# Kernel optimization log

Measured on AMD Instinct MI355X. Metric: run time of the kernel, lower is better.

Reference implementation:

```python
import jax, jax.numpy as jnp
import numpy as np

B, N, DIM = 2, 2048, 1024
NUM_HEADS = 16
EFF = NUM_HEADS // 2          # 8 effective heads
HD = DIM // NUM_HEADS         # 64
LAMBDA_INIT = 0.8
EPS = 1e-5


def setup_inputs() -> dict:
    key = jax.random.key(0)
    ks = jax.random.split(key, 16)
    s = 0.02
    return {
        "x":  jax.random.normal(ks[0], (B, N, DIM), dtype=jnp.float32),
        "Wq": jax.random.normal(ks[1], (DIM, DIM), dtype=jnp.float32) * s,
        "bq": jnp.zeros((DIM,), dtype=jnp.float32),
        "Wk": jax.random.normal(ks[2], (DIM, DIM), dtype=jnp.float32) * s,
        "bk": jnp.zeros((DIM,), dtype=jnp.float32),
        "Wv": jax.random.normal(ks[3], (DIM, DIM), dtype=jnp.float32) * s,
        "bv": jnp.zeros((DIM,), dtype=jnp.float32),
        "Wo": jax.random.normal(ks[4], (DIM, DIM), dtype=jnp.float32) * s,
        "bo": jnp.zeros((DIM,), dtype=jnp.float32),
        "norm_w": jnp.ones((2 * HD,), dtype=jnp.float32),
        "lq1": jax.random.normal(ks[5], (HD,), dtype=jnp.float32) * 0.1,
        "lk1": jax.random.normal(ks[6], (HD,), dtype=jnp.float32) * 0.1,
        "lq2": jax.random.normal(ks[7], (HD,), dtype=jnp.float32) * 0.1,
        "lk2": jax.random.normal(ks[8], (HD,), dtype=jnp.float32) * 0.1,
    }


def reference(x, Wq, bq, Wk, bk, Wv, bv, Wo, bo, norm_w, lq1, lk1, lq2, lk2):
    scale = HD ** -0.5
    # projections (torch Linear: y = x @ W.T + b)
    q = (x @ Wq.T + bq).reshape(B, N, NUM_HEADS, HD).transpose(0, 2, 1, 3) * scale  # [B,2E,N,hd]
    k = (x @ Wk.T + bk).reshape(B, N, NUM_HEADS, HD).transpose(0, 2, 1, 3)          # [B,2E,N,hd]
    v = (x @ Wv.T + bv).reshape(B, N, EFF, 2 * HD).transpose(0, 2, 1, 3)            # [B,E,N,2hd]

    scores = jnp.einsum('bhqd,bhkd->bhqk', q, k)              # [B,2E,N,N]
    probs = jax.nn.softmax(scores, axis=-1)
    probs = probs.reshape(B, EFF, 2, N, N)                    # pair consecutive heads

    lam = jnp.exp(jnp.sum(lq1 * lk1)) - jnp.exp(jnp.sum(lq2 * lk2)) + LAMBDA_INIT
    diff = probs[:, :, 0] - lam * probs[:, :, 1]              # [B,E,N,N]

    out = jnp.einsum('behk,bekd->behd'.replace('e','h').replace('hh','h') if False else 'bhqk,bhkd->bhqd', diff, v)  # [B,E,N,2hd]
    # headwise RMSNorm over last dim (2*hd)
    out = out * jax.lax.rsqrt(jnp.mean(out * out, axis=-1, keepdims=True) + EPS) * norm_w
    out = out * (1.0 - LAMBDA_INIT)

    out = out.transpose(0, 2, 1, 3).reshape(B, N, DIM)
    return out @ Wo.T + bo
```

## Files before the change

### kernel.cpp

```cpp
#include <hip/hip_runtime.h>
#include <hip/hip_bf16.h>

#define B_   2
#define N_   2048
#define DIM_ 1024
#define HD_  64
#define DV_  128

typedef __bf16 bf16;
typedef __bf16 bf16x8 __attribute__((ext_vector_type(8)));
typedef __bf16 bf16x4 __attribute__((ext_vector_type(4)));
typedef float  floatx4 __attribute__((ext_vector_type(4)));

#if __has_builtin(__builtin_amdgcn_exp2f)
#define EXP2(x) __builtin_amdgcn_exp2f(x)
#else
#define EXP2(x) exp2f(x)
#endif

#define QSCALE 0.1803368801111244f

__device__ __forceinline__ void async16(const void* g, void* l) {
  __builtin_amdgcn_global_load_lds(
      (__attribute__((address_space(1))) void*)g,
      (__attribute__((address_space(3))) void*)l, 16, 0, 0);
}

__global__ void convert_kernel(const float* __restrict__ x,
                               const float* __restrict__ wq,
                               const float* __restrict__ wk,
                               const float* __restrict__ wv,
                               const float* __restrict__ wo,
                               bf16* __restrict__ dst) {
  const int NX = B_ * N_ * DIM_;
  const int NW = DIM_ * DIM_;
  int i = (blockIdx.x * 256 + threadIdx.x) * 4;
  const float* src;
  int off;
  if (i < NX) { src = x; off = i; }
  else {
    int j = i - NX;
    int w = j >> 20;
    off = j & (NW - 1);
    src = (w == 0) ? wq : (w == 1) ? wk : (w == 2) ? wv : wo;
  }
  float4 v = *(const float4*)(src + off);
  bf16x4 o = { (bf16)v.x, (bf16)v.y, (bf16)v.z, (bf16)v.w };
  *(bf16x4*)(dst + i) = o;
}

__global__ void lam_kernel(const float* __restrict__ lq1, const float* __restrict__ lk1,
                           const float* __restrict__ lq2, const float* __restrict__ lk2,
                           float* __restrict__ lam_out) {
  int l = threadIdx.x;
  float a = lq1[l] * lk1[l];
  float b = lq2[l] * lk2[l];
  for (int m = 1; m < 64; m <<= 1) {
    a += __shfl_xor(a, m, 64);
    b += __shfl_xor(b, m, 64);
  }
  if (l == 0) *lam_out = __expf(a) - __expf(b) + 0.8f;
}

__global__ __launch_bounds__(256) void proj_kernel(
    const bf16* __restrict__ xb, const bf16* __restrict__ wall,
    const float* __restrict__ bq, const float* __restrict__ bk,
    const float* __restrict__ bv,
    bf16* __restrict__ qo, bf16* __restrict__ ko, bf16* __restrict__ vt) {
  __shared__ __align__(16) bf16 At[128 * 64];
  __shared__ __align__(16) bf16 Bt[128 * 64];
  const int tid = threadIdx.x, lane = tid & 63, w = tid >> 6;
  const int tm = blockIdx.x, tn = blockIdx.y, z = blockIdx.z;
  const int quad = lane >> 4, l15 = lane & 15;
  const int wm = (w >> 1) * 64, wn = (w & 1) * 64;
  const bf16* Ab = xb + (long)tm * 128 * DIM_;
  const bf16* Bb = wall + (long)z * (DIM_ * DIM_) + (long)tn * 128 * DIM_;
  floatx4 zero = {0.f, 0.f, 0.f, 0.f};
  floatx4 acc[4][4];
#pragma unroll
  for (int i = 0; i < 4; ++i)
#pragma unroll
    for (int j = 0; j < 4; ++j) acc[i][j] = zero;

  for (int kb = 0; kb < DIM_ / 64; ++kb) {
    for (int idx = tid; idx < 1024; idx += 256) {
      int row = idx >> 3, ch = idx & 7, g = ch ^ (row & 7);
      async16(Ab + row * DIM_ + kb * 64 + g * 8, (char*)At + (idx - lane) * 16);
      async16(Bb + row * DIM_ + kb * 64 + g * 8, (char*)Bt + (idx - lane) * 16);
    }
    __syncthreads();
#pragma unroll
    for (int ks = 0; ks < 2; ++ks) {
      bf16x8 af[4], bfm[4];
#pragma unroll
      for (int mt = 0; mt < 4; ++mt) {
        int r = wm + mt * 16 + l15;
        af[mt] = *(const bf16x8*)&At[r * 64 + ((ks * 4 + quad) ^ (r & 7)) * 8];
      }
#pragma unroll
      for (int nt = 0; nt < 4; ++nt) {
        int r = wn + nt * 16 + l15;
        bfm[nt] = *(const bf16x8*)&Bt[r * 64 + ((ks * 4 + quad) ^ (r & 7)) * 8];
      }
#pragma unroll
      for (int mt = 0; mt < 4; ++mt)
#pragma unroll
        for (int nt = 0; nt < 4; ++nt)
          acc[mt][nt] = __builtin_amdgcn_mfma_f32_16x16x32_bf16(
              af[mt], bfm[nt], acc[mt][nt], 0, 0, 0);
    }
    __syncthreads();
  }
#pragma unroll
  for (int mt = 0; mt < 4; ++mt)
#pragma unroll
    for (int nt = 0; nt < 4; ++nt)
#pragma unroll
      for (int r = 0; r < 4; ++r) {
        int grow = tm * 128 + wm + mt * 16 + quad * 4 + r;
        int gcol = tn * 128 + wn + nt * 16 + l15;
        float v = acc[mt][nt][r];
        if (z == 0) {
          qo[(long)grow * DIM_ + gcol] = (bf16)((v + bq[gcol]) * QSCALE);
        } else if (z == 1) {
          ko[(long)grow * DIM_ + gcol] = (bf16)(v + bk[gcol]);
        } else {
          int bb = grow >> 11, key = grow & (N_ - 1);
          int e = gcol >> 7, d = gcol & 127;
          vt[(((long)(bb * 8 + e)) * DV_ + d) * N_ + key] = (bf16)(v + bv[gcol]);
        }
      }
}

__global__ __launch_bounds__(256) void attn_kernel(
    const bf16* __restrict__ qb, const bf16* __restrict__ kbuf,
    const bf16* __restrict__ vt, float* __restrict__ O) {
  __shared__ __align__(16) bf16 Qt[64 * 64];
  __shared__ __align__(16) bf16 Kt[64 * 64];
  __shared__ __align__(16) bf16 Pt[64 * 64];
  __shared__ __align__(16) bf16 Vt[128 * 64];
  const int tid = threadIdx.x, lane = tid & 63, w = tid >> 6;
  const int qt = blockIdx.x, h = blockIdx.y, b = blockIdx.z, e = h >> 1;
  const int quad = lane >> 4, l15 = lane & 15;
  floatx4 zero = {0.f, 0.f, 0.f, 0.f};

  for (int idx = tid; idx < 512; idx += 256) {
    int row = idx >> 3, ch = idx & 7, g = ch ^ (row & 7);
    async16(qb + ((long)(b * N_ + qt * 64 + row)) * DIM_ + h * 64 + g * 8,
            (char*)Qt + (idx - lane) * 16);
  }
  __syncthreads();
  bf16x8 qf[2];
  {
    int ar = w * 16 + l15;
    qf[0] = *(const bf16x8*)&Qt[ar * 64 + ((quad) ^ (ar & 7)) * 8];
    qf[1] = *(const bf16x8*)&Qt[ar * 64 + ((4 + quad) ^ (ar & 7)) * 8];
  }

  floatx4 acc[8];
#pragma unroll
  for (int i = 0; i < 8; ++i) acc[i] = zero;
  float lpart[4] = {0.f, 0.f, 0.f, 0.f};

  for (int kt = 0; kt < N_ / 64; ++kt) {
    for (int idx = tid; idx < 512; idx += 256) {
      int row = idx >> 3, ch = idx & 7, g = ch ^ (row & 7);
      async16(kbuf + ((long)(b * N_ + kt * 64 + row)) * DIM_ + h * 64 + g * 8,
              (char*)Kt + (idx - lane) * 16);
    }
    for (int idx = tid; idx < 1024; idx += 256) {
      int row = idx >> 3, ch = idx & 7, g = ch ^ (row & 7);
      async16(vt + ((long)((b * 8 + e) * DV_ + row)) * N_ + kt * 64 + g * 8,
              (char*)Vt + (idx - lane) * 16);
    }
    __syncthreads();

    floatx4 s[4];
#pragma unroll
    for (int nt = 0; nt < 4; ++nt) s[nt] = zero;
#pragma unroll
    for (int ks = 0; ks < 2; ++ks) {
#pragma unroll
      for (int nt = 0; nt < 4; ++nt) {
        int br = nt * 16 + l15;
        bf16x8 bfm = *(const bf16x8*)&Kt[br * 64 + ((ks * 4 + quad) ^ (br & 7)) * 8];
        s[nt] = __builtin_amdgcn_mfma_f32_16x16x32_bf16(qf[ks], bfm, s[nt], 0, 0, 0);
      }
    }

#pragma unroll
    for (int r = 0; r < 4; ++r) {
      float p0 = EXP2(s[0][r]);
      float p1 = EXP2(s[1][r]);
      float p2 = EXP2(s[2][r]);
      float p3 = EXP2(s[3][r]);
      lpart[r] += (p0 + p1) + (p2 + p3);
      int row = w * 16 + quad * 4 + r;
      int k0 = l15;
      Pt[row * 64 + ((k0 >> 3) ^ (row & 7)) * 8 + (k0 & 7)] = (bf16)p0;
      int k1 = 16 + l15;
      Pt[row * 64 + ((k1 >> 3) ^ (row & 7)) * 8 + (k1 & 7)] = (bf16)p1;
      int k2 = 32 + l15;
      Pt[row * 64 + ((k2 >> 3) ^ (row & 7)) * 8 + (k2 & 7)] = (bf16)p2;
      int k3 = 48 + l15;
      Pt[row * 64 + ((k3 >> 3) ^ (row & 7)) * 8 + (k3 & 7)] = (bf16)p3;
    }

#pragma unroll
    for (int ks = 0; ks < 2; ++ks) {
      int ar = w * 16 + l15;
      bf16x8 af = *(const bf16x8*)&Pt[ar * 64 + ((ks * 4 + quad) ^ (ar & 7)) * 8];
#pragma unroll
      for (int dt = 0; dt < 8; ++dt) {
        int br = dt * 16 + l15;
        bf16x8 bfm = *(const bf16x8*)&Vt[br * 64 + ((ks * 4 + quad) ^ (br & 7)) * 8];
        acc[dt] = __builtin_amdgcn_mfma_f32_16x16x32_bf16(af, bfm, acc[dt], 0, 0, 0);
      }
    }
    __syncthreads();
  }

  float inv[4];
#pragma unroll
  for (int r = 0; r < 4; ++r) {
    float ls = lpart[r];
#pragma unroll
    for (int msk = 1; msk < 16; msk <<= 1) ls += __shfl_xor(ls, msk, 16);
    inv[r] = 1.0f / ls;
  }
#pragma unroll
  for (int dt = 0; dt < 8; ++dt)
#pragma unroll
    for (int r = 0; r < 4; ++r) {
      int q = qt * 64 + w * 16 + quad * 4 + r;
      int d = dt * 16 + l15;
      O[(((long)(b * 16 + h)) * N_ + q) * DV_ + d] = acc[dt][r] * inv[r];
    }
}

__global__ void combine_kernel(const float* __restrict__ O, const float* __restrict__ lamp,
                               const float* __restrict__ norm_w, bf16* __restrict__ ao) {
  int bid = blockIdx.x;
  int e = bid & 7, n = (bid >> 3) & (N_ - 1), b = bid >> 14;
  int lane = threadIdx.x;
  float lam = *lamp;
  const float* o1 = O + (((long)(b * 16 + 2 * e)) * N_ + n) * DV_;
  const float* o2 = O + (((long)(b * 16 + 2 * e + 1)) * N_ + n) * DV_;
  float d0 = o1[lane] - lam * o2[lane];
  float d1 = o1[lane + 64] - lam * o2[lane + 64];
  float ss = d0 * d0 + d1 * d1;
  for (int m = 1; m < 64; m <<= 1) ss += __shfl_xor(ss, m, 64);
  float r = rsqrtf(ss * (1.0f / 128.0f) + 1e-5f);
  float y0 = d0 * r * norm_w[lane] * 0.2f;
  float y1 = d1 * r * norm_w[lane + 64] * 0.2f;
  bf16* dst = ao + ((long)(b * N_ + n)) * DIM_ + e * DV_;
  dst[lane] = (bf16)y0;
  dst[lane + 64] = (bf16)y1;
}

__global__ __launch_bounds__(256) void out_gemm(
    const bf16* __restrict__ ab, const bf16* __restrict__ wo,
    const float* __restrict__ bo, float* __restrict__ out) {
  __shared__ __align__(16) bf16 At[128 * 64];
  __shared__ __align__(16) bf16 Bt[128 * 64];
  const int tid = threadIdx.x, lane = tid & 63, w = tid >> 6;
  const int tm = blockIdx.x, tn = blockIdx.y;
  const int quad = lane >> 4, l15 = lane & 15;
  const int wm = (w >> 1) * 64, wn = (w & 1) * 64;
  const bf16* Ab = ab + (long)tm * 128 * DIM_;
  const bf16* Bb = wo + (long)tn * 128 * DIM_;
  floatx4 zero = {0.f, 0.f, 0.f, 0.f};
  floatx4 acc[4][4];
#pragma unroll
  for (int i = 0; i < 4; ++i)
#pragma unroll
    for (int j = 0; j < 4; ++j) acc[i][j] = zero;

  for (int kb = 0; kb < DIM_ / 64; ++kb) {
    for (int idx = tid; idx < 1024; idx += 256) {
      int row = idx >> 3, ch = idx & 7, g = ch ^ (row & 7);
      async16(Ab + row * DIM_ + kb * 64 + g * 8, (char*)At + (idx - lane) * 16);
      async16(Bb + row * DIM_ + kb * 64 + g * 8, (char*)Bt + (idx - lane) * 16);
    }
    __syncthreads();
#pragma unroll
    for (int ks = 0; ks < 2; ++ks) {
      bf16x8 af[4], bfm[4];
#pragma unroll
      for (int mt = 0; mt < 4; ++mt) {
        int r = wm + mt * 16 + l15;
        af[mt] = *(const bf16x8*)&At[r * 64 + ((ks * 4 + quad) ^ (r & 7)) * 8];
      }
#pragma unroll
      for (int nt = 0; nt < 4; ++nt) {
        int r = wn + nt * 16 + l15;
        bfm[nt] = *(const bf16x8*)&Bt[r * 64 + ((ks * 4 + quad) ^ (r & 7)) * 8];
      }
#pragma unroll
      for (int mt = 0; mt < 4; ++mt)
#pragma unroll
        for (int nt = 0; nt < 4; ++nt)
          acc[mt][nt] = __builtin_amdgcn_mfma_f32_16x16x32_bf16(
              af[mt], bfm[nt], acc[mt][nt], 0, 0, 0);
    }
    __syncthreads();
  }
#pragma unroll
  for (int mt = 0; mt < 4; ++mt)
#pragma unroll
    for (int nt = 0; nt < 4; ++nt)
#pragma unroll
      for (int r = 0; r < 4; ++r) {
        int grow = tm * 128 + wm + mt * 16 + quad * 4 + r;
        int gcol = tn * 128 + wn + nt * 16 + l15;
        out[(long)grow * DIM_ + gcol] = acc[mt][nt][r] + bo[gcol];
      }
}

extern "C" void kernel_launch(void* const* d_in, const int* in_sizes, int n_in,
                              void* d_out, int out_size, void* d_ws, size_t ws_size,
                              hipStream_t stream) {
  const float* x    = (const float*)d_in[0];
  const float* Wq   = (const float*)d_in[1];
  const float* bq   = (const float*)d_in[2];
  const float* Wk   = (const float*)d_in[3];
  const float* bk   = (const float*)d_in[4];
  const float* Wv   = (const float*)d_in[5];
  const float* bv   = (const float*)d_in[6];
  const float* Wo   = (const float*)d_in[7];
  const float* bo   = (const float*)d_in[8];
  const float* nw   = (const float*)d_in[9];
  const float* lq1  = (const float*)d_in[10];
  const float* lk1  = (const float*)d_in[11];
  const float* lq2  = (const float*)d_in[12];
  const float* lk2  = (const float*)d_in[13];

  char* ws = (char*)d_ws;
  float* lam = (float*)ws;
  bf16* xb   = (bf16*)(ws + 256);
  bf16* wqb  = xb + 4194304;
  bf16* qb   = wqb + 4 * 1048576;
  bf16* kbuf = qb + 4194304;
  bf16* vtb  = kbuf + 4194304;
  bf16* ab   = vtb + 4194304;
  float* O   = (float*)(ab + 4194304);

  convert_kernel<<<8192, 256, 0, stream>>>(x, Wq, Wk, Wv, Wo, xb);
  lam_kernel<<<1, 64, 0, stream>>>(lq1, lk1, lq2, lk2, lam);
  proj_kernel<<<dim3(32, 8, 3), 256, 0, stream>>>(xb, wqb, bq, bk, bv, qb, kbuf, vtb);
  attn_kernel<<<dim3(32, 16, 2), 256, 0, stream>>>(qb, kbuf, vtb, O);
  combine_kernel<<<32768, 64, 0, stream>>>(O, lam, nw, ab);
  out_gemm<<<dim3(32, 8), 256, 0, stream>>>(ab, wqb + 3 * 1048576, bo, (float*)d_out);
}
```

Baseline: 254.5 us.

## Fuse head-pair attention with differential combine and RMSNorm epilogue

Each attention block now processes both heads of a differential pair, sharing one V tile load across them, and performs the lambda-weighted difference, RMSNorm and scaling in its epilogue, writing bf16 directly to the output-projection input. This removes the fp32 O intermediate write/read and the separate combine kernel launch, and halves V traffic. Q fragments are loaded straight from global, and per-wave P buffers are used. The cost is doubled accumulator registers (two sets of 8 floatx4), which may reduce occupancy, and half as many blocks in the grid.

```diff
diff --git a/kernel.cpp b/kernel.cpp
--- a/kernel.cpp
+++ b/kernel.cpp
@@ -132,130 +132,145 @@
       }
 }
 
-__global__ __launch_bounds__(256) void attn_kernel(
+__global__ __launch_bounds__(256, 2) void attn_kernel(
     const bf16* __restrict__ qb, const bf16* __restrict__ kbuf,
-    const bf16* __restrict__ vt, float* __restrict__ O) {
-  __shared__ __align__(16) bf16 Qt[64 * 64];
-  __shared__ __align__(16) bf16 Kt[64 * 64];
-  __shared__ __align__(16) bf16 Pt[64 * 64];
+    const bf16* __restrict__ vt, const float* __restrict__ lamp,
+    const float* __restrict__ norm_w, bf16* __restrict__ ao) {
+  __shared__ __align__(16) bf16 Kt[2 * 64 * 64];
   __shared__ __align__(16) bf16 Vt[128 * 64];
+  __shared__ __align__(16) bf16 Pt[4 * 16 * 64];
+
   const int tid = threadIdx.x, lane = tid & 63, w = tid >> 6;
-  const int qt = blockIdx.x, h = blockIdx.y, b = blockIdx.z, e = h >> 1;
+  const int qt = blockIdx.x, e = blockIdx.y, b = blockIdx.z;
   const int quad = lane >> 4, l15 = lane & 15;
   floatx4 zero = {0.f, 0.f, 0.f, 0.f};
 
-  for (int idx = tid; idx < 512; idx += 256) {
-    int row = idx >> 3, ch = idx & 7, g = ch ^ (row & 7);
-    async16(qb + ((long)(b * N_ + qt * 64 + row)) * DIM_ + h * 64 + g * 8,
-            (char*)Qt + (idx - lane) * 16);
-  }
-  __syncthreads();
-  bf16x8 qf[2];
-  {
-    int ar = w * 16 + l15;
-    qf[0] = *(const bf16x8*)&Qt[ar * 64 + ((quad) ^ (ar & 7)) * 8];
-    qf[1] = *(const bf16x8*)&Qt[ar * 64 + ((4 + quad) ^ (ar & 7)) * 8];
-  }
-
-  floatx4 acc[8];
-#pragma unroll
-  for (int i = 0; i < 8; ++i) acc[i] = zero;
-  float lpart[4] = {0.f, 0.f, 0.f, 0.f};
+  const int qrow = qt * 64 + w * 16 + l15;
+  const bf16* qrp = qb + (long)(b * N_ + qrow) * DIM_ + e * 128;
+  bf16x8 qf0[2], qf1[2];
+  qf0[0] = *(const bf16x8*)(qrp + quad * 8);
+  qf0[1] = *(const bf16x8*)(qrp + 32 + quad * 8);
+  qf1[0] = *(const bf16x8*)(qrp + 64 + quad * 8);
+  qf1[1] = *(const bf16x8*)(qrp + 96 + quad * 8);
+
+  floatx4 acc0[8], acc1[8];
+#pragma unroll
+  for (int i = 0; i < 8; ++i) { acc0[i] = zero; acc1[i] = zero; }
+  float lp0[4] = {0.f, 0.f, 0.f, 0.f};
+  float lp1[4] = {0.f, 0.f, 0.f, 0.f};
+
+  bf16* Ptw = Pt + w * 1024;
 
   for (int kt = 0; kt < N_ / 64; ++kt) {
-    for (int idx = tid; idx < 512; idx += 256) {
-      int row = idx >> 3, ch = idx & 7, g = ch ^ (row & 7);
-      async16(kbuf + ((long)(b * N_ + kt * 64 + row)) * DIM_ + h * 64 + g * 8,
+#pragma unroll
+    for (int t = 0; t < 4; ++t) {
+      int idx = tid + t * 256;
+      int khl = idx >> 9, row = (idx >> 3) & 63, ch = idx & 7, g = ch ^ (row & 7);
+      async16(kbuf + ((long)(b * N_ + kt * 64 + row)) * DIM_ + (e * 2 + khl) * 64 + g * 8,
               (char*)Kt + (idx - lane) * 16);
     }
-    for (int idx = tid; idx < 1024; idx += 256) {
+#pragma unroll
+    for (int t = 0; t < 4; ++t) {
+      int idx = tid + t * 256;
       int row = idx >> 3, ch = idx & 7, g = ch ^ (row & 7);
       async16(vt + ((long)((b * 8 + e) * DV_ + row)) * N_ + kt * 64 + g * 8,
               (char*)Vt + (idx - lane) * 16);
     }
     __syncthreads();
 
-    floatx4 s[4];
-#pragma unroll
-    for (int nt = 0; nt < 4; ++nt) s[nt] = zero;
-#pragma unroll
-    for (int ks = 0; ks < 2; ++ks) {
-#pragma unroll
-      for (int nt = 0; nt < 4; ++nt) {
-        int br = nt * 16 + l15;
-        bf16x8 bfm = *(const bf16x8*)&Kt[br * 64 + ((ks * 4 + quad) ^ (br & 7)) * 8];
-        s[nt] = __builtin_amdgcn_mfma_f32_16x16x32_bf16(qf[ks], bfm, s[nt], 0, 0, 0);
-      }
-    }
-
+#pragma unroll
+    for (int hl = 0; hl < 2; ++hl) {
+      const bf16* Kh = Kt + hl * 4096;
+      floatx4* acc = hl ? acc1 : acc0;
+      float* lp = hl ? lp1 : lp0;
+
+      floatx4 s[4];
+#pragma unroll
+      for (int nt = 0; nt < 4; ++nt) s[nt] = zero;
+#pragma unroll
+      for (int ks = 0; ks < 2; ++ks) {
+        bf16x8 qf = hl ? qf1[ks] : qf0[ks];
+#pragma unroll
+        for (int nt = 0; nt < 4; ++nt) {
+          int br = nt * 16 + l15;
+          bf16x8 bfm = *(const bf16x8*)&Kh[br * 64 + ((ks * 4 + quad) ^ (br & 7)) * 8];
+          s[nt] = __builtin_amdgcn_mfma_f32_16x16x32_bf16(qf, bfm, s[nt], 0, 0, 0);
+        }
+      }
+
+#pragma unroll
+      for (int r = 0; r < 4; ++r) {
+        float p0 = EXP2(s[0][r]);
+        float p1 = EXP2(s[1][r]);
+        float p2 = EXP2(s[2][r]);
+        float p3 = EXP2(s[3][r]);
+        lp[r] += (p0 + p1) + (p2 + p3);
+        int row = quad * 4 + r;
+        int k0 = l15;
+        Ptw[row * 64 + ((k0 >> 3) ^ (row & 7)) * 8 + (k0 & 7)] = (bf16)p0;
+        int k1 = 16 + l15;
+        Ptw[row * 64 + ((k1 >> 3) ^ (row & 7)) * 8 + (k1 & 7)] = (bf16)p1;
+        int k2 = 32 + l15;
+        Ptw[row * 64 + ((k2 >> 3) ^ (row & 7)) * 8 + (k2 & 7)] = (bf16)p2;
+        int k3 = 48 + l15;
+        Ptw[row * 64 + ((k3 >> 3) ^ (row & 7)) * 8 + (k3 & 7)] = (bf16)p3;
+      }
+
+#pragma unroll
+      for (int ks = 0; ks < 2; ++ks) {
+        bf16x8 af = *(const bf16x8*)&Ptw[l15 * 64 + ((ks * 4 + quad) ^ (l15 & 7)) * 8];
+#pragma unroll
+        for (int dt = 0; dt < 8; ++dt) {
+          int br = dt * 16 + l15;
+          bf16x8 bfm = *(const bf16x8*)&Vt[br * 64 + ((ks * 4 + quad) ^ (br & 7)) * 8];
+          acc[dt] = __builtin_amdgcn_mfma_f32_16x16x32_bf16(af, bfm, acc[dt], 0, 0, 0);
+        }
+      }
+    }
+    __syncthreads();
+  }
+
+  float inv0[4], inv1[4];
+#pragma unroll
+  for (int r = 0; r < 4; ++r) {
+    float a = lp0[r], c = lp1[r];
+#pragma unroll
+    for (int msk = 1; msk < 16; msk <<= 1) {
+      a += __shfl_xor(a, msk, 16);
+      c += __shfl_xor(c, msk, 16);
+    }
+    inv0[r] = 1.0f / a;
+    inv1[r] = 1.0f / c;
+  }
+
+  float lam = *lamp;
+  float ss[4] = {0.f, 0.f, 0.f, 0.f};
+#pragma unroll
+  for (int dt = 0; dt < 8; ++dt)
 #pragma unroll
     for (int r = 0; r < 4; ++r) {
-      float p0 = EXP2(s[0][r]);
-      float p1 = EXP2(s[1][r]);
-      float p2 = EXP2(s[2][r]);
-      float p3 = EXP2(s[3][r]);
-      lpart[r] += (p0 + p1) + (p2 + p3);
-      int row = w * 16 + quad * 4 + r;
-      int k0 = l15;
-      Pt[row * 64 + ((k0 >> 3) ^ (row & 7)) * 8 + (k0 & 7)] = (bf16)p0;
-      int k1 = 16 + l15;
-      Pt[row * 64 + ((k1 >> 3) ^ (row & 7)) * 8 + (k1 & 7)] = (bf16)p1;
-      int k2 = 32 + l15;
-      Pt[row * 64 + ((k2 >> 3) ^ (row & 7)) * 8 + (k2 & 7)] = (bf16)p2;
-      int k3 = 48 + l15;
-      Pt[row * 64 + ((k3 >> 3) ^ (row & 7)) * 8 + (k3 & 7)] = (bf16)p3;
-    }
-
-#pragma unroll
-    for (int ks = 0; ks < 2; ++ks) {
-      int ar = w * 16 + l15;
-      bf16x8 af = *(const bf16x8*)&Pt[ar * 64 + ((ks * 4 + quad) ^ (ar & 7)) * 8];
-#pragma unroll
-      for (int dt = 0; dt < 8; ++dt) {
-        int br = dt * 16 + l15;
-        bf16x8 bfm = *(const bf16x8*)&Vt[br * 64 + ((ks * 4 + quad) ^ (br & 7)) * 8];
-        acc[dt] = __builtin_amdgcn_mfma_f32_16x16x32_bf16(af, bfm, acc[dt], 0, 0, 0);
-      }
-    }
-    __syncthreads();
-  }
-
-  float inv[4];
+      float v = acc0[dt][r] * inv0[r] - lam * (acc1[dt][r] * inv1[r]);
+      acc0[dt][r] = v;
+      ss[r] += v * v;
+    }
+  float rms[4];
 #pragma unroll
   for (int r = 0; r < 4; ++r) {
-    float ls = lpart[r];
-#pragma unroll
-    for (int msk = 1; msk < 16; msk <<= 1) ls += __shfl_xor(ls, msk, 16);
-    inv[r] = 1.0f / ls;
-  }
-#pragma unroll
-  for (int dt = 0; dt < 8; ++dt)
+    float t = ss[r];
+#pragma unroll
+    for (int msk = 1; msk < 16; msk <<= 1) t += __shfl_xor(t, msk, 16);
+    rms[r] = rsqrtf(t * (1.0f / 128.0f) + 1e-5f);
+  }
+#pragma unroll
+  for (int dt = 0; dt < 8; ++dt) {
+    float nwv = norm_w[dt * 16 + l15] * 0.2f;
 #pragma unroll
     for (int r = 0; r < 4; ++r) {
-      int q = qt * 64 + w * 16 + quad * 4 + r;
-      int d = dt * 16 + l15;
-      O[(((long)(b * 16 + h)) * N_ + q) * DV_ + d] = acc[dt][r] * inv[r];
-    }
-}
-
-__global__ void combine_kernel(const float* __restrict__ O, const float* __restrict__ lamp,
-                               const float* __restrict__ norm_w, bf16* __restrict__ ao) {
-  int bid = blockIdx.x;
-  int e = bid & 7, n = (bid >> 3) & (N_ - 1), b = bid >> 14;
-  int lane = threadIdx.x;
-  float lam = *lamp;
-  const float* o1 = O + (((long)(b * 16 + 2 * e)) * N_ + n) * DV_;
-  const float* o2 = O + (((long)(b * 16 + 2 * e + 1)) * N_ + n) * DV_;
-  float d0 = o1[lane] - lam * o2[lane];
-  float d1 = o1[lane + 64] - lam * o2[lane + 64];
-  float ss = d0 * d0 + d1 * d1;
-  for (int m = 1; m < 64; m <<= 1) ss += __shfl_xor(ss, m, 64);
-  float r = rsqrtf(ss * (1.0f / 128.0f) + 1e-5f);
-  float y0 = d0 * r * norm_w[lane] * 0.2f;
-  float y1 = d1 * r * norm_w[lane + 64] * 0.2f;
-  bf16* dst = ao + ((long)(b * N_ + n)) * DIM_ + e * DV_;
-  dst[lane] = (bf16)y0;
-  dst[lane + 64] = (bf16)y1;
+      int n = qt * 64 + w * 16 + quad * 4 + r;
+      ao[((long)(b * N_ + n)) * DIM_ + e * DV_ + dt * 16 + l15] =
+          (bf16)(acc0[dt][r] * rms[r] * nwv);
+    }
+  }
 }
 
 __global__ __launch_bounds__(256) void out_gemm(
@@ -343,12 +358,10 @@
   bf16* kbuf = qb + 4194304;
   bf16* vtb  = kbuf + 4194304;
   bf16* ab   = vtb + 4194304;
-  float* O   = (float*)(ab + 4194304);
 
   convert_kernel<<<8192, 256, 0, stream>>>(x, Wq, Wk, Wv, Wo, xb);
   lam_kernel<<<1, 64, 0, stream>>>(lq1, lk1, lq2, lk2, lam);
   proj_kernel<<<dim3(32, 8, 3), 256, 0, stream>>>(xb, wqb, bq, bk, bv, qb, kbuf, vtb);
-  attn_kernel<<<dim3(32, 16, 2), 256, 0, stream>>>(qb, kbuf, vtb, O);
-  combine_kernel<<<32768, 64, 0, stream>>>(O, lam, nw, ab);
+  attn_kernel<<<dim3(32, 8, 2), 256, 0, stream>>>(qb, kbuf, vtb, lam, nw, ab);
   out_gemm<<<dim3(32, 8), 256, 0, stream>>>(ab, wqb + 3 * 1048576, bo, (float*)d_out);
 }
```

Result: faster. 244.7 us (-3.8%).
